# Optimization experiments

Hardware: AMD Instinct MI355X
Metric: run time of the kernel (lower is better)

The kernel has to match this reference:

```python
import jax, jax.numpy as jnp
import numpy as np

_R = 15            # OpenCV bilateralFilter radius = d//2 for d=31
_SIG_COLOR = 75.0
_SIG_SPACE = 15.0
_BN_EPS = 1e-5

def _bilateral_tables():
    # circular neighborhood with precomputed spatial Gaussian weights (OpenCV style)
    offs, sws = [], []
    for dx in range(-_R, _R + 1):
        for dy in range(-_R, _R + 1):
            r2 = dx * dx + dy * dy
            if r2 > _R * _R:
                continue
            offs.append((dx, dy))
            sws.append(np.exp(-0.5 * r2 / (_SIG_SPACE ** 2)))
    return np.asarray(offs, np.int32), np.asarray(sws, np.float32)

def bilateral_filter(gray):
    # gray: [B,H,W] float32 holding uint8-valued pixels in [0,255]
    B, H, W = gray.shape
    offs, sws = _bilateral_tables()
    pad = jnp.pad(gray, ((0, 0), (_R, _R), (_R, _R)), mode='reflect')  # BORDER_REFLECT_101
    inv2sc2 = -0.5 / (_SIG_COLOR ** 2)

    def step(carry, inp):
        num, den = carry
        off, sw = inp
        sh = jax.lax.dynamic_slice(pad, (0, _R + off[0], _R + off[1]), (B, H, W))
        d = sh - gray
        w = sw * jnp.exp(inv2sc2 * d * d)
        return (num + w * sh, den + w), None

    init = (jnp.zeros_like(gray), jnp.zeros_like(gray))
    (num, den), _ = jax.lax.scan(step, init, (jnp.asarray(offs), jnp.asarray(sws)))
    return jnp.round(num / den)  # mimic uint8 rounding of cv2 output

# Effective integer offsets produced by int(i + cos(2*pi*p/8)) / int(j - sin(...))
# truncation in the original loop (radius=1, n_points=8). Note p=7 compares the
# center with itself (bit 128 always set) -- faithful to the source's math.
_LBP_OFFS = [(1, 0), (0, -1), (0, -1), (-1, -1), (-1, 0), (-1, 0), (0, 1), (0, 0)]

def compute_lbp(img):
    # img: [B,H,W]; interior pixels only, border stays 0 (as in source)
    B, H, W = img.shape
    c = img[:, 1:H - 1, 1:W - 1]
    pat = jnp.zeros_like(c)
    for p, (dx, dy) in enumerate(_LBP_OFFS):
        n = img[:, 1 + dx:H - 1 + dx, 1 + dy:W - 1 + dy]
        pat = pat + (2.0 ** p) * (n >= c).astype(c.dtype)
    return jnp.zeros((B, H, W), img.dtype).at[:, 1:H - 1, 1:W - 1].set(pat)

def _texture(img):
    # grayscale with the source's (buggy but faithful) 0.116 blue weight
    gray = 0.299 * img[:, 0] + 0.587 * img[:, 1] + 0.116 * img[:, 2]
    q = jnp.clip(jnp.floor(gray * 255.0), 0.0, 255.0)  # (gray*255).astype(uint8)
    filt = bilateral_filter(q)
    return compute_lbp(filt) / 255.0

def _conv(x, w, b):
    y = jax.lax.conv_general_dilated(x, w, (1, 1), ((1, 1), (1, 1)),
                                     dimension_numbers=('NCHW', 'OIHW', 'NCHW'))
    return y + b.reshape(1, -1, 1, 1)

def _bn(x, g, b):
    # training-mode BatchNorm (fresh module): batch statistics over (N,H,W)
    m = jnp.mean(x, (0, 2, 3), keepdims=True)
    v = jnp.var(x, (0, 2, 3), keepdims=True)
    return g.reshape(1, -1, 1, 1) * (x - m) * jax.lax.rsqrt(v + _BN_EPS) + b.reshape(1, -1, 1, 1)

def setup_inputs() -> dict:
    key = jax.random.key(0)
    ks = jax.random.split(key, 5)
    img = jax.random.uniform(ks[0], (8, 3, 256, 256), dtype=jnp.float32)
    w1 = jax.random.normal(ks[1], (32, 1, 3, 3), dtype=jnp.float32) / 3.0
    b1 = jax.random.normal(ks[2], (32,), dtype=jnp.float32) * 0.05
    w2 = jax.random.normal(ks[3], (64, 32, 3, 3), dtype=jnp.float32) / jnp.sqrt(32.0 * 9.0)
    b2 = jax.random.normal(ks[4], (64,), dtype=jnp.float32) * 0.05
    return {'img': img,
            'w1': w1, 'b1': b1, 'g1': jnp.ones((32,), jnp.float32), 'beta1': jnp.zeros((32,), jnp.float32),
            'w2': w2, 'b2': b2, 'g2': jnp.ones((64,), jnp.float32), 'beta2': jnp.zeros((64,), jnp.float32)}

def reference(img, w1, b1, g1, beta1, w2, b2, g2, beta2):
    lbp = jax.lax.stop_gradient(_texture(img))[:, None]  # [B,1,H,W]; source detaches input
    x = jax.nn.relu(_bn(_conv(lbp, w1, b1), g1, beta1))
    x = jax.nn.relu(_bn(_conv(x, w2, b2), g2, beta2))
    x = jax.lax.reduce_window(x, -jnp.inf, jax.lax.max, (1, 1, 2, 2), (1, 1, 2, 2), 'VALID')
    return x
```

## Files before the change

kernel.cpp:

```cpp
#include <hip/hip_runtime.h>
#include <math.h>

#define RAD 15
#define DIAM 31

typedef unsigned char u8;
typedef unsigned short ushort_t;
typedef __attribute__((ext_vector_type(8))) short bf16x8;
typedef __attribute__((ext_vector_type(4))) float f32x4;

__device__ __forceinline__ unsigned short f2bf(float f){
  unsigned u = __float_as_uint(f);
  return (unsigned short)((u + 0x7FFFu + ((u >> 16) & 1u)) >> 16);
}

__global__ __launch_bounds__(256) void k_gp(const float* __restrict__ img, u8* __restrict__ q,
                                            const float* __restrict__ w2, ushort_t* __restrict__ w2b,
                                            float* __restrict__ wc_g, float* __restrict__ swt_g){
  int blk = blockIdx.x, tid = threadIdx.x;
  if (blk < 2048){
    int i = blk*256 + tid;
    int b = i >> 16, p = i & 65535;
    const float* pb = img + (((size_t)b*3) << 16);
    float r = pb[p], g = pb[65536 + p], bl = pb[131072 + p];
    float gray = __fadd_rn(__fadd_rn(__fmul_rn(0.299f, r), __fmul_rn(0.587f, g)), __fmul_rn(0.116f, bl));
    float t = floorf(__fmul_rn(gray, 255.0f));
    t = fminf(fmaxf(t, 0.0f), 255.0f);
    q[i] = (u8)(int)t;
  } else if (blk < 2120){
    int i = (blk - 2048)*256 + tid;
    int j = i & 7, l = (i >> 3) & 63, fo = i >> 9;
    int t = fo >> 2, o = fo & 3;
    int oc = o*16 + (l & 15), ic = (l >> 4)*8 + j;
    w2b[i] = f2bf(w2[(oc*32 + ic)*9 + t]);
  } else {
    const float inv2sc2 = (float)(-0.5/5625.0);
    float df = (float)tid;
    float t = __fmul_rn(__fmul_rn(inv2sc2, df), df);
    wc_g[tid] = (float)exp((double)t);
    for (int i = tid; i < DIAM*DIAM; i += 256){
      int dx = i / DIAM - RAD, dy = i % DIAM - RAD;
      int r2 = dx*dx + dy*dy;
      swt_g[i] = (r2 <= RAD*RAD) ? (float)exp(-0.5 * (double)r2 / 225.0) : 0.0f;
    }
  }
}

__global__ __launch_bounds__(256) void k_bilateral(const u8* __restrict__ q, u8* __restrict__ filt,
                                                   const float* __restrict__ wc_g,
                                                   const float* __restrict__ swt_g){
  __shared__ __align__(16) u8 sm[32768 + 62*68];
  float* wcr  = (float*)sm;
  u8*   tileB = sm + 32768;
  int b = blockIdx.z;
  int gx0 = blockIdx.x * 32, gy0 = blockIdx.y * 32;
  int tid = threadIdx.x;
  const u8* qb = q + ((size_t)b << 16);
  {
    float v = wc_g[tid];
    float4 v4 = make_float4(v, v, v, v);
    #pragma unroll
    for (int k = 0; k < 8; ++k) *(float4*)&wcr[tid*32 + k*4] = v4;
  }
  for (int i = tid; i < 62*62; i += 256){
    int ly = i / 62, lx = i % 62;
    int gy = gy0 + ly - RAD, gx = gx0 + lx - RAD;
    gy = gy < 0 ? -gy : (gy > 255 ? 510 - gy : gy);
    gx = gx < 0 ? -gx : (gx > 255 ? 510 - gx : gx);
    tileB[ly*68 + lx] = qb[(gy << 8) + gx];
  }
  __syncthreads();
  int tx8 = tid & 7, r = tid >> 3;
  int lk = (tid & 31);
  int cbase = (r + RAD)*68 + RAD + 4*tx8;
  float c_f[4], num[4], den[4];
  #pragma unroll
  for (int p = 0; p < 4; ++p){
    c_f[p] = (float)tileB[cbase + p];
    num[p] = 0.f; den[p] = 0.f;
  }
  #pragma unroll 1
  for (int dx = -RAD; dx <= RAD; ++dx){
    int dxx = dx*dx;
    int rowoff = (r + dx + RAD)*68 + 4*tx8;
    unsigned wrow[9];
    #pragma unroll
    for (int k = 0; k < 9; ++k) wrow[k] = *(const unsigned*)(tileB + rowoff + 4*k);
    const float* swrow = swt_g + (dx + RAD)*DIAM + RAD;
    #pragma unroll
    for (int DY = -RAD; DY <= RAD; ++DY){
      if (dxx + DY*DY <= RAD*RAD){
        float sw = swrow[DY];
        #pragma unroll
        for (int p = 0; p < 4; ++p){
          const int B = RAD + p + DY;
          float shf = (float)((wrow[B >> 2] >> ((B & 3)*8)) & 255u);
          float diff = __fsub_rn(shf, c_f[p]);
          int idx = (int)fabsf(diff);
          float wcd = wcr[(idx << 5) + lk];
          float w = __fmul_rn(sw, wcd);
          num[p] = __fadd_rn(num[p], __fmul_rn(w, shf));
          den[p] = __fadd_rn(den[p], w);
        }
      }
    }
  }
  unsigned pack = 0;
  #pragma unroll
  for (int p = 0; p < 4; ++p)
    pack |= ((unsigned)(int)rintf(__fdiv_rn(num[p], den[p]))) << (p*8);
  int gy = gy0 + r, gx = gx0 + 4*tx8;
  *(unsigned*)(filt + ((size_t)b << 16) + (gy << 8) + gx) = pack;
}

template<int OC>
__device__ __forceinline__ void block_stats(const float* acc, float* red, int tid, float* out){
  #pragma unroll
  for (int c0 = 0; c0 < OC; c0 += 8){
    #pragma unroll
    for (int pass = 0; pass < 2; ++pass){
      __syncthreads();
      #pragma unroll
      for (int j = 0; j < 8; ++j){
        float v = acc[c0 + j];
        red[tid*8 + j] = pass ? __fmul_rn(v, v) : v;
      }
      __syncthreads();
      int i = tid >> 5, s = tid & 31;
      float v = 0.f;
      #pragma unroll
      for (int k = 0; k < 8; ++k) v += red[(s + 32*k)*8 + i];
      v += __shfl_xor(v, 1); v += __shfl_xor(v, 2); v += __shfl_xor(v, 4);
      v += __shfl_xor(v, 8); v += __shfl_xor(v, 16);
      if (s == 0) out[2*(c0 + i) + pass] = v;
    }
  }
}

__global__ __launch_bounds__(256) void k_lbp1(const u8* __restrict__ filt, const float* __restrict__ w1,
                                              u8* __restrict__ lbp, float* __restrict__ part1){
  __shared__ u8    ft[20][20];
  __shared__ float lt[18][18];
  __shared__ float wl[288];
  __shared__ float red[2048];
  int b = blockIdx.z;
  int ty0 = blockIdx.y * 16, tx0 = blockIdx.x * 16;
  int tid = threadIdx.x, tx = tid & 15, ty = tid >> 4;
  for (int i = tid; i < 288; i += 256) wl[i] = w1[i];
  for (int i = tid; i < 400; i += 256){
    int iy = i / 20, ix = i % 20;
    int gy = ty0 + iy - 2, gx = tx0 + ix - 2;
    u8 v = 0;
    if ((unsigned)gy < 256u && (unsigned)gx < 256u) v = filt[((size_t)b << 16) + (gy << 8) + gx];
    ft[iy][ix] = v;
  }
  __syncthreads();
  for (int i = tid; i < 324; i += 256){
    int jy = i / 18, jx = i % 18;
    int gy = ty0 + jy - 1, gx = tx0 + jx - 1;
    int pat = 0;
    if (gy > 0 && gy < 255 && gx > 0 && gx < 255){
      int c = ft[jy+1][jx+1];
      pat = 128;
      pat += (ft[jy+2][jx+1] >= c) ? 1  : 0;
      pat += (ft[jy+1][jx  ] >= c) ? 6  : 0;
      pat += (ft[jy  ][jx  ] >= c) ? 8  : 0;
      pat += (ft[jy  ][jx+1] >= c) ? 48 : 0;
      pat += (ft[jy+1][jx+2] >= c) ? 64 : 0;
    }
    lt[jy][jx] = __fdiv_rn((float)pat, 255.0f);
    if (jy >= 1 && jy <= 16 && jx >= 1 && jx <= 16 && (unsigned)gy < 256u && (unsigned)gx < 256u)
      lbp[((size_t)b << 16) + (gy << 8) + gx] = (u8)pat;
  }
  __syncthreads();
  float v[9];
  #pragma unroll
  for (int j = 0; j < 9; ++j) v[j] = lt[ty + j/3][tx + j%3];
  float acc[32];
  #pragma unroll
  for (int oc = 0; oc < 32; ++oc){
    float a = 0.f;
    #pragma unroll
    for (int j = 0; j < 9; ++j) a = fmaf(v[j], wl[oc*9 + j], a);
    acc[oc] = a;
  }
  int blk = (blockIdx.z * 16 + blockIdx.y) * 16 + blockIdx.x;
  block_stats<32>(acc, red, tid, part1 + (size_t)blk * 64);
}

__global__ __launch_bounds__(256) void k_stats(const float* __restrict__ part, int stride, int OC,
                                               const float* __restrict__ g, const float* __restrict__ beta,
                                               float* __restrict__ st){
  int ch = blockIdx.x, tid = threadIdx.x;
  double s = 0.0, s2 = 0.0;
  for (int k = tid; k < 2048; k += 256){
    const float* pp = part + (size_t)k * stride + 2*ch;
    s += (double)pp[0]; s2 += (double)pp[1];
  }
  #pragma unroll
  for (int m = 1; m <= 32; m <<= 1){ s += __shfl_xor(s, m); s2 += __shfl_xor(s2, m); }
  __shared__ double red[8];
  if ((tid & 63) == 0){ red[(tid >> 6)*2] = s; red[(tid >> 6)*2 + 1] = s2; }
  __syncthreads();
  if (tid == 0){
    s  = red[0] + red[2] + red[4] + red[6];
    s2 = red[1] + red[3] + red[5] + red[7];
    double mean = s / 524288.0;
    double var  = s2 / 524288.0 - mean*mean;
    double rs   = 1.0 / sqrt(var + 1e-5);
    double sc   = (double)g[ch] * rs;
    st[ch]      = (float)sc;
    st[OC + ch] = (float)((double)beta[ch] - mean * sc);
  }
}

#define SM_Y1   0
#define SM_LT   25920
#define SM_WL   27520
#define SM_RED  25920
__global__ __launch_bounds__(256) void k_fused(const u8* __restrict__ lbp, const float* __restrict__ w1,
                                               const ushort_t* __restrict__ w2b,
                                               const float* __restrict__ st1,
                                               float* __restrict__ part2, float* __restrict__ out){
  __shared__ __align__(16) u8 smem[28672];
  ushort_t* y1h = (ushort_t*)(smem + SM_Y1);
  float*    lt  = (float*)(smem + SM_LT);
  float*    wl  = (float*)(smem + SM_WL);
  int b = blockIdx.z;
  int ty0 = blockIdx.y * 16, tx0 = blockIdx.x * 16;
  int tid = threadIdx.x;
  for (int i = tid; i < 288; i += 256) wl[i] = w1[i];
  for (int i = tid; i < 400; i += 256){
    int iy = i / 20, ix = i % 20;
    int gy = ty0 + iy - 2, gx = tx0 + ix - 2;
    float v = 0.f;
    if ((unsigned)gy < 256u && (unsigned)gx < 256u)
      v = __fdiv_rn((float)lbp[((size_t)b << 16) + (gy << 8) + gx], 255.0f);
    lt[i] = v;
  }
  __syncthreads();
  for (int i = tid; i < 324; i += 256){
    int jy = i / 18, jx = i % 18;
    int gy = ty0 + jy - 1, gx = tx0 + jx - 1;
    bool in = ((unsigned)gy < 256u) && ((unsigned)gx < 256u);
    float v[9];
    #pragma unroll
    for (int j = 0; j < 9; ++j) v[j] = lt[(jy + j/3)*20 + jx + j%3];
    ushort_t* row = y1h + i*40;
    #pragma unroll
    for (int o4 = 0; o4 < 4; ++o4){
      unsigned tmp[4];
      #pragma unroll
      for (int j2 = 0; j2 < 4; ++j2){
        int oc = o4*8 + j2*2;
        float a0 = 0.f, a1 = 0.f;
        #pragma unroll
        for (int j = 0; j < 9; ++j){
          a0 = fmaf(v[j], wl[(oc  )*9 + j], a0);
          a1 = fmaf(v[j], wl[(oc+1)*9 + j], a1);
        }
        float r0 = in ? fmaxf(fmaf(a0, st1[oc  ], st1[32 + oc  ]), 0.f) : 0.f;
        float r1 = in ? fmaxf(fmaf(a1, st1[oc+1], st1[32 + oc+1]), 0.f) : 0.f;
        tmp[j2] = (unsigned)f2bf(r0) | ((unsigned)f2bf(r1) << 16);
      }
      *(uint4*)(row + o4*8) = make_uint4(tmp[0], tmp[1], tmp[2], tmp[3]);
    }
  }
  __syncthreads();
  int lane = tid & 63, w = tid >> 6;
  int mA = lane & 15, g = lane >> 4;
  int pyA = mA >> 2, pxA = mA & 3;
  f32x4 acc[4][4] = {};
  #pragma unroll 3
  for (int t = 0; t < 9; ++t){
    int dy = t/3, dx = t%3;
    bf16x8 bf[4];
    #pragma unroll
    for (int o = 0; o < 4; ++o) bf[o] = *(const bf16x8*)(w2b + (((t*4 + o) << 6) + lane)*8);
    #pragma unroll
    for (int i = 0; i < 4; ++i){
      int jy = (w << 2) + pyA + dy, jx = (i << 2) + pxA + dx;
      bf16x8 a = *(const bf16x8*)(y1h + (jy*18 + jx)*40 + g*8);
      #pragma unroll
      for (int o = 0; o < 4; ++o)
        acc[i][o] = __builtin_amdgcn_mfma_f32_16x16x32_bf16(a, bf[o], acc[i][o], 0, 0, 0);
    }
  }
  int col = lane & 15;
  {
    float* red = (float*)(smem + SM_RED);
    float s[4], s2[4];
    #pragma unroll
    for (int o = 0; o < 4; ++o){
      s[o] = 0.f; s2[o] = 0.f;
      #pragma unroll
      for (int i = 0; i < 4; ++i)
        #pragma unroll
        for (int rr = 0; rr < 4; ++rr){
          float v = acc[i][o][rr];
          s[o] += v; s2[o] = fmaf(v, v, s2[o]);
        }
      s[o]  += __shfl_xor(s[o], 16);  s[o]  += __shfl_xor(s[o], 32);
      s2[o] += __shfl_xor(s2[o], 16); s2[o] += __shfl_xor(s2[o], 32);
    }
    if (g == 0){
      #pragma unroll
      for (int o = 0; o < 4; ++o){
        red[((0*4 + w)*4 + o)*16 + col] = s[o];
        red[((1*4 + w)*4 + o)*16 + col] = s2[o];
      }
    }
    __syncthreads();
    if (tid < 128){
      int stat = tid >> 6, oc = tid & 63, o = oc >> 4, c = oc & 15;
      float* red2 = (float*)(smem + SM_RED);
      float sum = 0.f;
      #pragma unroll
      for (int ww = 0; ww < 4; ++ww) sum += red2[((stat*4 + ww)*4 + o)*16 + c];
      int blk = (blockIdx.z * 16 + blockIdx.y) * 16 + blockIdx.x;
      part2[(size_t)blk * 128 + 2*oc + stat] = sum;
    }
  }
  {
    float* pool = (float*)(smem + SM_Y1);
    #pragma unroll
    for (int o = 0; o < 4; ++o){
      int oc = (o << 4) + col;
      #pragma unroll
      for (int i = 0; i < 4; ++i){
        float h0 = fmaxf(acc[i][o][0], acc[i][o][1]);
        float h2 = fmaxf(acc[i][o][2], acc[i][o][3]);
        float p0 = fmaxf(h0, __shfl_xor(h0, 16));
        float p2 = fmaxf(h2, __shfl_xor(h2, 16));
        if (!(g & 1)){
          *(float2*)&pool[oc*66 + (w*2 + (g >> 1))*8 + i*2] = make_float2(p0, p2);
        }
      }
    }
    __syncthreads();
    int Y0 = blockIdx.y * 8, X0 = blockIdx.x * 8;
    for (int k = tid; k < 1024; k += 256){
      int oc = k >> 4, quad = k & 15;
      int row = quad >> 1, c4 = (quad & 1) * 4;
      float4 v = *(float4*)&pool[oc*66 + quad*4];
      *(float4*)&out[(((size_t)b*64 + oc) << 14) + (size_t)(Y0 + row)*128 + X0 + c4] = v;
    }
  }
}

__global__ __launch_bounds__(256) void k_bn2(float* __restrict__ out, const float* __restrict__ st2){
  int i = blockIdx.x*256 + threadIdx.x;
  int oc = (i >> 12) & 63;
  float sc = st2[oc], sh = st2[64 + oc];
  float4 v = ((float4*)out)[i];
  v.x = fmaxf(fmaf(v.x, sc, sh), 0.f);
  v.y = fmaxf(fmaf(v.y, sc, sh), 0.f);
  v.z = fmaxf(fmaf(v.z, sc, sh), 0.f);
  v.w = fmaxf(fmaf(v.w, sc, sh), 0.f);
  ((float4*)out)[i] = v;
}

extern "C" void kernel_launch(void* const* d_in, const int* in_sizes, int n_in,
                              void* d_out, int out_size, void* d_ws, size_t ws_size,
                              hipStream_t stream){
  const float* img = (const float*)d_in[0];
  const float* w1  = (const float*)d_in[1];
  const float* g1  = (const float*)d_in[3];
  const float* be1 = (const float*)d_in[4];
  const float* w2  = (const float*)d_in[5];
  const float* g2  = (const float*)d_in[7];
  const float* be2 = (const float*)d_in[8];
  float* out = (float*)d_out;

  char* base = (char*)d_ws;
  u8*       q    = (u8*)(base + 0);
  u8*       filt = (u8*)(base + 524288);
  u8*       lbp  = (u8*)(base + 1048576);
  ushort_t* w2b  = (ushort_t*)(base + 1572864);
  float*    wc_g = (float*)(base + 1609728);
  float*    swtg = (float*)(base + 1610752);
  float*    p1   = (float*)(base + 1614608);
  float*    p2   = (float*)(base + 2138896);
  float*    st1  = (float*)(base + 3187472);
  float*    st2  = (float*)(base + 3187728);

  k_gp       <<<2121, 256, 0, stream>>>(img, q, w2, w2b, wc_g, swtg);
  k_bilateral<<<dim3(8,8,8), 256, 0, stream>>>(q, filt, wc_g, swtg);
  k_lbp1     <<<dim3(16,16,8), 256, 0, stream>>>(filt, w1, lbp, p1);
  k_stats    <<<32, 256, 0, stream>>>(p1, 64, 32, g1, be1, st1);
  k_fused    <<<dim3(16,16,8), 256, 0, stream>>>(lbp, w1, w2b, st1, p2, out);
  k_stats    <<<64, 256, 0, stream>>>(p2, 128, 64, g2, be2, st2);
  k_bn2      <<<8192, 256, 0, stream>>>(out, st2);
}
```

Before: 203.9 us.

## Split bilateral work to two pixels per thread and use inline-asm arithmetic

Each block of the bilateral kernel now covers 32x16 output pixels instead of 32x32. Each thread computes 2 pixels instead of 4, which doubles the grid to 1024 blocks and raises parallelism and occupancy. The inner arithmetic uses inline asm for sub, mul, fmac and add, so the compiler cannot reorder or fuse these operations. The cost is a larger halo overhead relative to the tile and repeated row loads per thread. The fmac also changes rounding compared with the separate mul and add used before.

```diff
diff --git a/kernel.cpp b/kernel.cpp
--- a/kernel.cpp
+++ b/kernel.cpp
@@ -13,6 +13,11 @@
   unsigned u = __float_as_uint(f);
   return (unsigned short)((u + 0x7FFFu + ((u >> 16) & 1u)) >> 16);
 }
+
+__device__ __forceinline__ float asub(float a, float b){ float d; asm("v_sub_f32 %0, %1, %2" : "=v"(d) : "v"(a), "v"(b)); return d; }
+__device__ __forceinline__ float amul(float a, float b){ float d; asm("v_mul_f32 %0, %1, %2" : "=v"(d) : "v"(a), "v"(b)); return d; }
+__device__ __forceinline__ void  aacc(float& acc, float v){ asm("v_add_f32 %0, %0, %1" : "+v"(acc) : "v"(v)); }
+__device__ __forceinline__ void  afma(float& acc, float a, float b){ asm("v_fmac_f32 %0, %1, %2" : "+v"(acc) : "v"(a), "v"(b)); }
 
 __global__ __launch_bounds__(256) void k_gp(const float* __restrict__ img, u8* __restrict__ q,
                                             const float* __restrict__ w2, ushort_t* __restrict__ w2b,
@@ -46,14 +51,53 @@
   }
 }
 
+template<int BASE>
+__device__ __forceinline__ void bil_body(const u8* tileB, const float* wcr, const float* swt_g,
+                                         int r, int tx8, int lk, float c0, float c1,
+                                         float& num0, float& den0, float& num1, float& den1){
+  #pragma unroll 1
+  for (int dx = -RAD; dx <= RAD; ++dx){
+    int dxx = dx*dx;
+    int rowoff = (r + dx + RAD)*68 + 4*tx8;
+    unsigned wrow[9];
+    #pragma unroll
+    for (int k = 0; k < 9; ++k) wrow[k] = *(const unsigned*)(tileB + rowoff + 4*k);
+    const float* swrow = swt_g + (dx + RAD)*DIAM + RAD;
+    #pragma unroll
+    for (int DY = -RAD; DY <= RAD; ++DY){
+      if (dxx + DY*DY <= RAD*RAD){
+        float sw = swrow[DY];
+        {
+          const int B = BASE + 0 + DY;
+          float shf = (float)((wrow[B >> 2] >> ((B & 3)*8)) & 255u);
+          float diff = asub(shf, c0);
+          int idx = (int)fabsf(diff);
+          float w = amul(sw, wcr[(idx << 5) + lk]);
+          afma(num0, w, shf);
+          aacc(den0, w);
+        }
+        {
+          const int B = BASE + 1 + DY;
+          float shf = (float)((wrow[B >> 2] >> ((B & 3)*8)) & 255u);
+          float diff = asub(shf, c1);
+          int idx = (int)fabsf(diff);
+          float w = amul(sw, wcr[(idx << 5) + lk]);
+          afma(num1, w, shf);
+          aacc(den1, w);
+        }
+      }
+    }
+  }
+}
+
 __global__ __launch_bounds__(256) void k_bilateral(const u8* __restrict__ q, u8* __restrict__ filt,
                                                    const float* __restrict__ wc_g,
                                                    const float* __restrict__ swt_g){
-  __shared__ __align__(16) u8 sm[32768 + 62*68];
+  __shared__ __align__(16) u8 sm[32768 + 46*68];
   float* wcr  = (float*)sm;
   u8*   tileB = sm + 32768;
   int b = blockIdx.z;
-  int gx0 = blockIdx.x * 32, gy0 = blockIdx.y * 32;
+  int gx0 = blockIdx.x * 32, gy0 = blockIdx.y * 16;
   int tid = threadIdx.x;
   const u8* qb = q + ((size_t)b << 16);
   {
@@ -62,7 +106,7 @@
     #pragma unroll
     for (int k = 0; k < 8; ++k) *(float4*)&wcr[tid*32 + k*4] = v4;
   }
-  for (int i = tid; i < 62*62; i += 256){
+  for (int i = tid; i < 46*62; i += 256){
     int ly = i / 62, lx = i % 62;
     int gy = gy0 + ly - RAD, gx = gx0 + lx - RAD;
     gy = gy < 0 ? -gy : (gy > 255 ? 510 - gy : gy);
@@ -70,47 +114,19 @@
     tileB[ly*68 + lx] = qb[(gy << 8) + gx];
   }
   __syncthreads();
-  int tx8 = tid & 7, r = tid >> 3;
-  int lk = (tid & 31);
-  int cbase = (r + RAD)*68 + RAD + 4*tx8;
-  float c_f[4], num[4], den[4];
-  #pragma unroll
-  for (int p = 0; p < 4; ++p){
-    c_f[p] = (float)tileB[cbase + p];
-    num[p] = 0.f; den[p] = 0.f;
-  }
-  #pragma unroll 1
-  for (int dx = -RAD; dx <= RAD; ++dx){
-    int dxx = dx*dx;
-    int rowoff = (r + dx + RAD)*68 + 4*tx8;
-    unsigned wrow[9];
-    #pragma unroll
-    for (int k = 0; k < 9; ++k) wrow[k] = *(const unsigned*)(tileB + rowoff + 4*k);
-    const float* swrow = swt_g + (dx + RAD)*DIAM + RAD;
-    #pragma unroll
-    for (int DY = -RAD; DY <= RAD; ++DY){
-      if (dxx + DY*DY <= RAD*RAD){
-        float sw = swrow[DY];
-        #pragma unroll
-        for (int p = 0; p < 4; ++p){
-          const int B = RAD + p + DY;
-          float shf = (float)((wrow[B >> 2] >> ((B & 3)*8)) & 255u);
-          float diff = __fsub_rn(shf, c_f[p]);
-          int idx = (int)fabsf(diff);
-          float wcd = wcr[(idx << 5) + lk];
-          float w = __fmul_rn(sw, wcd);
-          num[p] = __fadd_rn(num[p], __fmul_rn(w, shf));
-          den[p] = __fadd_rn(den[p], w);
-        }
-      }
-    }
-  }
-  unsigned pack = 0;
-  #pragma unroll
-  for (int p = 0; p < 4; ++p)
-    pack |= ((unsigned)(int)rintf(__fdiv_rn(num[p], den[p]))) << (p*8);
-  int gy = gy0 + r, gx = gx0 + 4*tx8;
-  *(unsigned*)(filt + ((size_t)b << 16) + (gy << 8) + gx) = pack;
+  int tx8 = tid & 7, rr = tid >> 3;
+  int r = rr & 15, ph = rr >> 4;
+  int lk = tid & 31;
+  int cbase = (r + RAD)*68 + RAD + 4*tx8 + 2*ph;
+  float c0 = (float)tileB[cbase + 0];
+  float c1 = (float)tileB[cbase + 1];
+  float num0 = 0.f, den0 = 0.f, num1 = 0.f, den1 = 0.f;
+  if (ph == 0) bil_body<15>(tileB, wcr, swt_g, r, tx8, lk, c0, c1, num0, den0, num1, den1);
+  else         bil_body<17>(tileB, wcr, swt_g, r, tx8, lk, c0, c1, num0, den0, num1, den1);
+  unsigned p0 = (unsigned)(int)rintf(__fdiv_rn(num0, den0));
+  unsigned p1 = (unsigned)(int)rintf(__fdiv_rn(num1, den1));
+  int gy = gy0 + r, gx = gx0 + 4*tx8 + 2*ph;
+  *(ushort_t*)(filt + ((size_t)b << 16) + (gy << 8) + gx) = (ushort_t)(p0 | (p1 << 8));
 }
 
 template<int OC>
@@ -385,7 +401,7 @@
   float*    st2  = (float*)(base + 3187728);
 
   k_gp       <<<2121, 256, 0, stream>>>(img, q, w2, w2b, wc_g, swtg);
-  k_bilateral<<<dim3(8,8,8), 256, 0, stream>>>(q, filt, wc_g, swtg);
+  k_bilateral<<<dim3(8,16,8), 256, 0, stream>>>(q, filt, wc_g, swtg);
   k_lbp1     <<<dim3(16,16,8), 256, 0, stream>>>(filt, w1, lbp, p1);
   k_stats    <<<32, 256, 0, stream>>>(p1, 64, 32, g1, be1, st1);
   k_fused    <<<dim3(16,16,8), 256, 0, stream>>>(lbp, w1, w2b, st1, p2, out);
```

Result: faster. 196.6 us (-3.6%).
